# Optimization experiments

Measured on AMD Instinct MI355X. Metric: run time of the kernel, lower is better.

The kernel has to match this reference:

```python
import jax, jax.numpy as jnp
import numpy as np


def grid_sample_bilinear(img, grid):
    """Replicates torch F.grid_sample(mode='bilinear', padding_mode='zeros',
    align_corners=False). img: [B,C,Hin,Win]; grid: [B,Ho,Wo,2] in [-1,1]
    with grid[...,0]=x (width), grid[...,1]=y (height). Returns [B,C,Ho,Wo]."""
    B, C, Hin, Win = img.shape
    x = (grid[..., 0] + 1.0) * (Win * 0.5) - 0.5  # unnormalized pixel coords
    y = (grid[..., 1] + 1.0) * (Hin * 0.5) - 0.5
    x0 = jnp.floor(x)
    y0 = jnp.floor(y)
    wx1 = x - x0
    wy1 = y - y0

    def tap(xi, yi, w):
        valid = ((xi >= 0) & (xi < Win) & (yi >= 0) & (yi < Hin)).astype(img.dtype)
        xc = jnp.clip(xi, 0, Win - 1).astype(jnp.int32)
        yc = jnp.clip(yi, 0, Hin - 1).astype(jnp.int32)
        def gather_one(im, yb, xb, wb):
            return im[:, yb, xb] * wb[None]  # [C,Ho,Wo]
        return jax.vmap(gather_one)(img, yc, xc, valid * w)

    return (tap(x0, y0, (1.0 - wx1) * (1.0 - wy1))
            + tap(x0 + 1.0, y0, wx1 * (1.0 - wy1))
            + tap(x0, y0 + 1.0, (1.0 - wx1) * wy1)
            + tap(x0 + 1.0, y0 + 1.0, wx1 * wy1))


def setup_inputs() -> dict:
    key = jax.random.key(0)
    k_uv, k1, k2, k3, k4 = jax.random.split(key, 5)
    W, H = 2048, 2048
    B, Ho, Wo = 8, 1024, 1024
    return {
        "uv": jax.random.uniform(k_uv, (B, Ho, Wo, 2), dtype=jnp.float32),
        "layer1": jax.random.normal(k1, (1, 1, W, H), dtype=jnp.float32),
        "layer2": jax.random.normal(k2, (1, 1, W // 2, H // 2), dtype=jnp.float32),
        "layer3": jax.random.normal(k3, (1, 1, W // 4, H // 4), dtype=jnp.float32),
        "layer4": jax.random.normal(k4, (1, 1, W // 8, H // 8), dtype=jnp.float32),
    }


def reference(uv, layer1, layer2, layer3, layer4):
    B = uv.shape[0]
    grid = uv * 2.0 - 1.0
    y = None
    for layer in (layer1, layer2, layer3, layer4):
        img = jnp.broadcast_to(layer, (B,) + layer.shape[1:])  # repeat(B,1,1,1)
        s = grid_sample_bilinear(img, grid)
        y = s if y is None else y + s
    return y  # [B,1,Ho,Wo]
```

## Files before the change

### kernel.cpp

```cpp
#include <hip/hip_runtime.h>
#include <hip/hip_fp16.h>


typedef unsigned int u32x2 __attribute__((ext_vector_type(2)));
typedef unsigned int u32x4 __attribute__((ext_vector_type(4)));
typedef float f32x4 __attribute__((ext_vector_type(4)));

#define K 1024
#define CHUNK 4096
#define HB 4096
#define SEG (CHUNK * 256)
#define NXCD 8

__device__ __forceinline__ int binof(float u, float v) {
    int bx = min(max((int)(u * 32.0f), 0), 31);
    int by = min(max((int)(v * 32.0f), 0), 31);
    return by * 32 + bx;
}

__global__ __launch_bounds__(256) void repack_hist_kernel(
    const float* __restrict__ l1, const float* __restrict__ l2,
    const float* __restrict__ l3, const float* __restrict__ l4,
    __half2* __restrict__ r1, __half2* __restrict__ r2,
    __half2* __restrict__ r3, __half2* __restrict__ r4,
    const float2* __restrict__ uv, unsigned* __restrict__ hist, int n) {
    const int n1 = 2048 * 2048, n2 = 1024 * 1024, n3 = 512 * 512, n4 = 256 * 256;
    int i = blockIdx.x * 256 + threadIdx.x;
    {
        const float* __restrict__ src = nullptr;
        __half2* __restrict__ dst = nullptr;
        int S = 0, logS = 0, j = 0;
        if (i < n1) {
            src = l1; dst = r1; S = 2048; logS = 11; j = i;
        } else if (i < n1 + n2) {
            src = l2; dst = r2; S = 1024; logS = 10; j = i - n1;
        } else if (i < n1 + n2 + n3) {
            src = l3; dst = r3; S = 512; logS = 9; j = i - (n1 + n2);
        } else if (i < n1 + n2 + n3 + n4) {
            src = l4; dst = r4; S = 256; logS = 8; j = i - (n1 + n2 + n3);
        }
        if (src) {
            int y = j >> logS;
            float a = src[j];
            float b = src[(y < S - 1) ? (j + S) : j];
            dst[j] = __halves2half2(__float2half(a), __float2half(b));
        }
    }
    if (hist == nullptr) return;
    int base = blockIdx.x * HB;
    if (base >= n) return;
    __shared__ unsigned cnt[K];
    for (int b = threadIdx.x; b < K; b += 256) cnt[b] = 0u;
    __syncthreads();
    int m = min(HB, n - base);
    const f32x4* uv4 = (const f32x4*)(uv + base);
    int npair = m >> 1;
    for (int k2 = threadIdx.x; k2 < npair; k2 += 256) {
        f32x4 q = __builtin_nontemporal_load(&uv4[k2]);
        atomicAdd(&cnt[binof(q.x, q.y)], 1u);
        atomicAdd(&cnt[binof(q.z, q.w)], 1u);
    }
    if ((m & 1) && threadIdx.x == 0) {
        float2 q = uv[base + m - 1];
        atomicAdd(&cnt[binof(q.x, q.y)], 1u);
    }
    __syncthreads();
    int seg = base / SEG;
    unsigned* gh = hist + (size_t)seg * K;
    for (int b = threadIdx.x; b < K; b += 256) {
        unsigned v = cnt[b];
        if (v) atomicAdd(&gh[b], v);
    }
}

__global__ __launch_bounds__(256) void partition_kernel(
    const float2* __restrict__ uv, const unsigned* __restrict__ hist,
    unsigned* __restrict__ cursor, float2* __restrict__ uv_s,
    unsigned* __restrict__ invp, unsigned* __restrict__ idxp, int n,
    int pinned) {
    __shared__ float2 suv[CHUNK];
    __shared__ unsigned short slid[CHUNK];
    __shared__ unsigned cnt[K];
    __shared__ unsigned lbase[K];
    __shared__ unsigned goff[K];
    __shared__ unsigned part[256];
    int t = threadIdx.x;
    int blk = blockIdx.x;
    int c = pinned ? ((blk % NXCD) * (SEG / CHUNK) + blk / NXCD) : blk;
    int cb = c * CHUNK;
    if (cb >= n) return;
    int cnum = min(CHUNK, n - cb);
    int seg = cb / SEG;
    unsigned segstart = (unsigned)((size_t)seg * SEG);

    {
        const f32x4* uv4 = (const f32x4*)(uv + cb);
        int npair = cnum >> 1;
        for (int k2 = t; k2 < npair; k2 += 256) {
            f32x4 q = uv4[k2];
            suv[k2 * 2] = make_float2(q.x, q.y);
            suv[k2 * 2 + 1] = make_float2(q.z, q.w);
        }
        if ((cnum & 1) && t == 0) suv[cnum - 1] = uv[cb + cnum - 1];
    }
    for (int b = t; b < K; b += 256) cnt[b] = 0u;
    __syncthreads();
    for (int k = t; k < cnum; k += 256)
        atomicAdd(&cnt[binof(suv[k].x, suv[k].y)], 1u);
    __syncthreads();
    {
        unsigned v0 = cnt[t * 4], v1 = cnt[t * 4 + 1], v2 = cnt[t * 4 + 2],
                 v3 = cnt[t * 4 + 3];
        unsigned s1 = v0, s2 = v0 + v1, s3 = v0 + v1 + v2;
        part[t] = s3 + v3;
        __syncthreads();
        for (int off = 1; off < 256; off <<= 1) {
            unsigned x = (t >= off) ? part[t - off] : 0u;
            __syncthreads();
            part[t] += x;
            __syncthreads();
        }
        unsigned tb = (t > 0) ? part[t - 1] : 0u;
        lbase[t * 4] = tb;
        lbase[t * 4 + 1] = tb + s1;
        lbase[t * 4 + 2] = tb + s2;
        lbase[t * 4 + 3] = tb + s3;
    }
    __syncthreads();
    {
        const unsigned* h = hist + (size_t)seg * K;
        unsigned v0 = h[t * 4], v1 = h[t * 4 + 1], v2 = h[t * 4 + 2],
                 v3 = h[t * 4 + 3];
        unsigned s1 = v0, s2 = v0 + v1, s3 = v0 + v1 + v2;
        part[t] = s3 + v3;
        __syncthreads();
        for (int off = 1; off < 256; off <<= 1) {
            unsigned x = (t >= off) ? part[t - off] : 0u;
            __syncthreads();
            part[t] += x;
            __syncthreads();
        }
        unsigned tb = (t > 0) ? part[t - 1] : 0u;
        unsigned sbv[4] = {tb, tb + s1, tb + s2, tb + s3};
        for (int j = 0; j < 4; ++j) {
            int b = t * 4 + j;
            unsigned cc = cnt[b];
            unsigned r = cc ? atomicAdd(&cursor[(size_t)seg * K + b], cc) : 0u;
            goff[b] = segstart + sbv[j] + r;
        }
    }
    __syncthreads();
    for (int b = t; b < K; b += 256) cnt[b] = 0u;
    __syncthreads();
    for (int k = t; k < cnum; k += 256) {
        int b = binof(suv[k].x, suv[k].y);
        unsigned r = atomicAdd(&cnt[b], 1u);
        slid[lbase[b] + r] = (unsigned short)k;
        if (invp) invp[cb + k] = goff[b] + r;
    }
    __syncthreads();
    for (int s = t; s < cnum; s += 256) {
        int lid = slid[s];
        float2 q = suv[lid];
        int b = binof(q.x, q.y);
        unsigned pos = goff[b] + ((unsigned)s - lbase[b]);
        uv_s[pos] = q;
        if (idxp) idxp[pos] = (unsigned)(cb + lid);
    }
}

__device__ __forceinline__ float sample_level(const __half2* __restrict__ R,
                                              const int S, const float gx,
                                              const float gy) {
    const float halfS = 0.5f * (float)S;
    float x = (gx + 1.0f) * halfS - 0.5f;
    float y = (gy + 1.0f) * halfS - 0.5f;
    float xf = floorf(x), yf = floorf(y);
    float wx = x - xf, wy = y - yf;
    int x0 = (int)xf, y0 = (int)yf;

    int yc = min(max(y0, 0), S - 1);
    float wa = (y0 >= 0) ? (1.0f - wy) : wy;
    if (y0 < -1 || y0 >= S) wa = 0.0f;
    float wb = (y0 >= 0 && y0 < S - 1) ? wy : 0.0f;

    int xb = min(max(x0, 0), S - 2);
    bool xin = (x0 >= 0) && (x0 <= S - 2);
    float wxa = xin ? (1.0f - wx) : ((x0 == -1) ? wx : 0.0f);
    float wxb = xin ? wx : ((x0 == S - 1) ? (1.0f - wx) : 0.0f);

    uint2 q;
    __builtin_memcpy(&q, (const char*)(R + (size_t)yc * (size_t)S + xb), 8);
    __half2 ca = *(const __half2*)&q.x;
    __half2 cb = *(const __half2*)&q.y;
    float2 fa = __half22float2(ca);
    float2 fb = __half22float2(cb);
    float cola = fmaf(wa, fa.x, wb * fa.y);
    float colb = fmaf(wa, fb.x, wb * fb.y);
    return fmaf(wxa, cola, wxb * colb);
}

__device__ __forceinline__ float sample_point(const __half2* __restrict__ r1,
                                              const __half2* __restrict__ r2,
                                              const __half2* __restrict__ r3,
                                              const __half2* __restrict__ r4,
                                              float ux, float uy) {
    float gx = ux * 2.0f - 1.0f;
    float gy = uy * 2.0f - 1.0f;
    float acc = sample_level(r1, 2048, gx, gy);
    acc += sample_level(r2, 1024, gx, gy);
    acc += sample_level(r3, 512, gx, gy);
    acc += sample_level(r4, 256, gx, gy);
    return acc;
}

__global__ __launch_bounds__(256) void lappyr_sample4(
    const float2* __restrict__ uv_s, const __half2* __restrict__ r1,
    const __half2* __restrict__ r2, const __half2* __restrict__ r3,
    const __half2* __restrict__ r4, float* __restrict__ val_s, int n,
    int pinned) {
    int blk = blockIdx.x;
    int sb = pinned ? ((blk % NXCD) * (SEG / 1024) + blk / NXCD) : blk;
    int base = sb * 1024 + threadIdx.x * 4;
    if (base + 3 < n) {
        const f32x4* u4 = (const f32x4*)(uv_s + base);
        f32x4 a = __builtin_nontemporal_load(u4);
        f32x4 b = __builtin_nontemporal_load(u4 + 1);
        f32x4 res;
        res.x = sample_point(r1, r2, r3, r4, a.x, a.y);
        res.y = sample_point(r1, r2, r3, r4, a.z, a.w);
        res.z = sample_point(r1, r2, r3, r4, b.x, b.y);
        res.w = sample_point(r1, r2, r3, r4, b.z, b.w);
        *(f32x4*)(val_s + base) = res;
    } else {
        for (int j = 0; j < 4; ++j) {
            int p = base + j;
            if (p < n) {
                float2 q = uv_s[p];
                val_s[p] = sample_point(r1, r2, r3, r4, q.x, q.y);
            }
        }
    }
}

__global__ __launch_bounds__(256) void lappyr_unsort4(
    const unsigned* __restrict__ inv, const float* __restrict__ val_s,
    float* __restrict__ out, int n, int pinned) {
    int blk = blockIdx.x;
    int sb = pinned ? ((blk % NXCD) * (SEG / 1024) + blk / NXCD) : blk;
    int base = sb * 1024 + threadIdx.x * 4;
    if (base + 3 < n) {
        u32x4 iv = __builtin_nontemporal_load((const u32x4*)(inv + base));
        f32x4 res;
        res.x = val_s[iv.x];
        res.y = val_s[iv.y];
        res.z = val_s[iv.z];
        res.w = val_s[iv.w];
        __builtin_nontemporal_store(res, (f32x4*)(out + base));
    } else {
        for (int j = 0; j < 4; ++j) {
            int p = base + j;
            if (p < n) out[p] = val_s[inv[p]];
        }
    }
}

__global__ __launch_bounds__(256) void lappyr_sample_sorted(
    const float2* __restrict__ uv_s, const unsigned* __restrict__ idx_s,
    const __half2* __restrict__ r1, const __half2* __restrict__ r2,
    const __half2* __restrict__ r3, const __half2* __restrict__ r4,
    float* __restrict__ out, int n, int pinned) {
    int blk = blockIdx.x;
    int sb = pinned ? ((blk % NXCD) * (SEG / 512) + blk / NXCD) : blk;
    int i = sb * 256 + threadIdx.x;
    int p0 = i * 2;
    if (p0 >= n) return;
    if (p0 + 1 < n) {
        f32x4 q = __builtin_nontemporal_load((const f32x4*)uv_s + i);
        u32x2 id = __builtin_nontemporal_load((const u32x2*)idx_s + i);
        float a0 = sample_point(r1, r2, r3, r4, q.x, q.y);
        float a1 = sample_point(r1, r2, r3, r4, q.z, q.w);
        out[id.x] = a0;
        out[id.y] = a1;
    } else {
        float2 q = uv_s[p0];
        out[idx_s[p0]] = sample_point(r1, r2, r3, r4, q.x, q.y);
    }
}

__global__ __launch_bounds__(256) void lappyr_sample_kernel(
    const float2* __restrict__ uv, const __half2* __restrict__ r1,
    const __half2* __restrict__ r2, const __half2* __restrict__ r3,
    const __half2* __restrict__ r4, float* __restrict__ out, int n) {
    int i = blockIdx.x * blockDim.x + threadIdx.x;
    if (i >= n) return;
    float2 p = uv[i];
    out[i] = sample_point(r1, r2, r3, r4, p.x, p.y);
}

__device__ __forceinline__ float bilin_f32(const float* __restrict__ img,
                                           const int S, const float gx,
                                           const float gy) {
    const float halfS = 0.5f * (float)S;
    float x = (gx + 1.0f) * halfS - 0.5f;
    float y = (gy + 1.0f) * halfS - 0.5f;
    float xf = floorf(x), yf = floorf(y);
    float wx = x - xf, wy = y - yf;
    int x0 = (int)xf, y0 = (int)yf, x1 = x0 + 1, y1 = y0 + 1;
    float ex0 = (x0 >= 0 && x0 < S) ? (1.0f - wx) : 0.0f;
    float ex1 = (x1 >= 0 && x1 < S) ? wx : 0.0f;
    float ey0 = (y0 >= 0 && y0 < S) ? (1.0f - wy) : 0.0f;
    float ey1 = (y1 >= 0 && y1 < S) ? wy : 0.0f;
    int xc0 = min(max(x0, 0), S - 1), xc1 = min(max(x1, 0), S - 1);
    int yc0 = min(max(y0, 0), S - 1), yc1 = min(max(y1, 0), S - 1);
    const float* r0 = img + (size_t)yc0 * S;
    const float* r1 = img + (size_t)yc1 * S;
    return ey0 * fmaf(ex0, r0[xc0], ex1 * r0[xc1]) +
           ey1 * fmaf(ex0, r1[xc0], ex1 * r1[xc1]);
}

__global__ __launch_bounds__(256) void lappyr_f32_kernel(
    const float2* __restrict__ uv, const float* __restrict__ l1,
    const float* __restrict__ l2, const float* __restrict__ l3,
    const float* __restrict__ l4, float* __restrict__ out, int n) {
    int i = blockIdx.x * blockDim.x + threadIdx.x;
    if (i >= n) return;
    float2 p = uv[i];
    float gx = p.x * 2.0f - 1.0f;
    float gy = p.y * 2.0f - 1.0f;
    float acc = bilin_f32(l1, 2048, gx, gy);
    acc += bilin_f32(l2, 1024, gx, gy);
    acc += bilin_f32(l3, 512, gx, gy);
    acc += bilin_f32(l4, 256, gx, gy);
    out[i] = acc;
}

extern "C" void kernel_launch(void* const* d_in, const int* in_sizes, int n_in,
                              void* d_out, int out_size, void* d_ws, size_t ws_size,
                              hipStream_t stream) {
    const float2* uv = (const float2*)d_in[0];
    const float* l1 = (const float*)d_in[1];
    const float* l2 = (const float*)d_in[2];
    const float* l3 = (const float*)d_in[3];
    const float* l4 = (const float*)d_in[4];
    float* out = (float*)d_out;
    int n = out_size;

    const size_t n1 = 2048u * 2048u, n2 = 1024u * 1024u, n3 = 512u * 512u,
                 n4 = 256u * 256u;
    const size_t ntot = n1 + n2 + n3 + n4;
    const size_t rep_bytes = ntot * sizeof(__half2);

    int nseg = (n + SEG - 1) / SEG;
    size_t tbl_bytes = (size_t)nseg * K * 4 * 2;

    size_t off_uvs = (rep_bytes + 255) & ~(size_t)255;
    size_t off_inv = off_uvs + (size_t)n * 8;
    size_t off_val = off_inv + (size_t)n * 4;
    size_t off_hist2 = (off_val + (size_t)n * 4 + 255) & ~(size_t)255;
    size_t need2 = off_hist2 + tbl_bytes;
    size_t off_idx = off_uvs + (size_t)n * 8;
    size_t off_hist1 = (off_idx + (size_t)n * 4 + 255) & ~(size_t)255;
    size_t need1 = off_hist1 + tbl_bytes;

    int repack_blocks = (int)((ntot + 255) / 256);

    if (ws_size >= rep_bytes) {
        char* ws = (char*)d_ws;
        __half2* r1 = (__half2*)ws;
        __half2* r2 = r1 + n1;
        __half2* r3 = r2 + n2;
        __half2* r4 = r3 + n3;
        int pinned = (n == NXCD * SEG) ? 1 : 0;
        int hist_blocks = (n + HB - 1) / HB;
        int ga = max(repack_blocks, hist_blocks);
        int nchunks = (n + CHUNK - 1) / CHUNK;
        if (ws_size >= need2 && n > 0) {
            float2* uv_s = (float2*)(ws + off_uvs);
            unsigned* inv = (unsigned*)(ws + off_inv);
            float* val_s = (float*)(ws + off_val);
            unsigned* hist = (unsigned*)(ws + off_hist2);
            unsigned* cursor = hist + (size_t)nseg * K;
            hipMemsetAsync(ws + off_hist2, 0, tbl_bytes, stream);
            repack_hist_kernel<<<ga, 256, 0, stream>>>(l1, l2, l3, l4, r1, r2, r3,
                                                       r4, uv, hist, n);
            partition_kernel<<<nchunks, 256, 0, stream>>>(
                uv, hist, cursor, uv_s, inv, nullptr, n, pinned);
            int nb4 = (n + 1023) / 1024;
            lappyr_sample4<<<nb4, 256, 0, stream>>>(uv_s, r1, r2, r3, r4, val_s,
                                                    n, pinned);
            lappyr_unsort4<<<nb4, 256, 0, stream>>>(inv, val_s, out, n, pinned);
        } else if (ws_size >= need1 && n > 0) {
            float2* uv_s = (float2*)(ws + off_uvs);
            unsigned* idx_s = (unsigned*)(ws + off_idx);
            unsigned* hist = (unsigned*)(ws + off_hist1);
            unsigned* cursor = hist + (size_t)nseg * K;
            hipMemsetAsync(ws + off_hist1, 0, tbl_bytes, stream);
            repack_hist_kernel<<<ga, 256, 0, stream>>>(l1, l2, l3, l4, r1, r2, r3,
                                                       r4, uv, hist, n);
            partition_kernel<<<nchunks, 256, 0, stream>>>(
                uv, hist, cursor, uv_s, nullptr, idx_s, n, pinned);
            int nh = (n + 1) / 2;
            lappyr_sample_sorted<<<(nh + 255) / 256, 256, 0, stream>>>(
                uv_s, idx_s, r1, r2, r3, r4, out, n, pinned);
        } else {
            repack_hist_kernel<<<repack_blocks, 256, 0, stream>>>(
                l1, l2, l3, l4, r1, r2, r3, r4, uv, nullptr, n);
            lappyr_sample_kernel<<<(n + 255) / 256, 256, 0, stream>>>(
                uv, r1, r2, r3, r4, out, n);
        }
    } else {
        lappyr_f32_kernel<<<(n + 255) / 256, 256, 0, stream>>>(uv, l1, l2, l3, l4,
                                                               out, n);
    }
}
```

Before: 312.5 us.

## Precompute segment bin offsets with a scan kernel and streamline partition

Adds a per-segment scan kernel that turns the global histogram into starting cursors, so the partition kernel no longer rescans the histogram itself. The partition kernel now counts straight from global uv, scatters full uv pairs into a shared sorted buffer and writes the inverse permutation as vector stores. This removes the extra shared-memory uv copy and the local-id indirection. It costs one extra kernel launch and a second global read of uv per chunk.

```diff
diff --git a/kernel.cpp b/kernel.cpp
--- a/kernel.cpp
+++ b/kernel.cpp
@@ -73,11 +73,121 @@
     }
 }
 
+__global__ __launch_bounds__(256) void scan_kernel(
+    const unsigned* __restrict__ hist, unsigned* __restrict__ cursor) {
+    int seg = blockIdx.x;
+    const unsigned* h = hist + (size_t)seg * K;
+    unsigned* c = cursor + (size_t)seg * K;
+    __shared__ unsigned part[256];
+    int t = threadIdx.x;
+    unsigned v0 = h[t * 4], v1 = h[t * 4 + 1], v2 = h[t * 4 + 2], v3 = h[t * 4 + 3];
+    unsigned s1 = v0, s2 = v0 + v1, s3 = v0 + v1 + v2;
+    part[t] = s3 + v3;
+    __syncthreads();
+    for (int off = 1; off < 256; off <<= 1) {
+        unsigned x = (t >= off) ? part[t - off] : 0u;
+        __syncthreads();
+        part[t] += x;
+        __syncthreads();
+    }
+    unsigned tb = (t > 0) ? part[t - 1] : 0u;
+    unsigned segstart = (unsigned)((size_t)seg * SEG);
+    c[t * 4] = segstart + tb;
+    c[t * 4 + 1] = segstart + tb + s1;
+    c[t * 4 + 2] = segstart + tb + s2;
+    c[t * 4 + 3] = segstart + tb + s3;
+}
+
 __global__ __launch_bounds__(256) void partition_kernel(
+    const float2* __restrict__ uv, unsigned* __restrict__ cursor,
+    float2* __restrict__ uv_s, unsigned* __restrict__ invp, int n, int pinned) {
+    __shared__ float2 ssort[CHUNK];
+    __shared__ unsigned cnt[K];
+    __shared__ unsigned lbase[K];
+    __shared__ unsigned gdiff[K];
+    __shared__ unsigned part[256];
+    int t = threadIdx.x;
+    int blk = blockIdx.x;
+    int c = pinned ? ((blk % NXCD) * (SEG / CHUNK) + blk / NXCD) : blk;
+    int cb = c * CHUNK;
+    if (cb >= n) return;
+    int cnum = min(CHUNK, n - cb);
+    int seg = cb / SEG;
+
+    for (int b = t; b < K; b += 256) cnt[b] = 0u;
+    __syncthreads();
+    const f32x4* uv4 = (const f32x4*)(uv + cb);
+    int npair = cnum >> 1;
+    for (int k2 = t; k2 < npair; k2 += 256) {
+        f32x4 q = uv4[k2];
+        atomicAdd(&cnt[binof(q.x, q.y)], 1u);
+        atomicAdd(&cnt[binof(q.z, q.w)], 1u);
+    }
+    if ((cnum & 1) && t == 0) {
+        float2 q = uv[cb + cnum - 1];
+        atomicAdd(&cnt[binof(q.x, q.y)], 1u);
+    }
+    __syncthreads();
+    {
+        unsigned v0 = cnt[t * 4], v1 = cnt[t * 4 + 1], v2 = cnt[t * 4 + 2],
+                 v3 = cnt[t * 4 + 3];
+        unsigned s1 = v0, s2 = v0 + v1, s3 = v0 + v1 + v2;
+        part[t] = s3 + v3;
+        __syncthreads();
+        for (int off = 1; off < 256; off <<= 1) {
+            unsigned x = (t >= off) ? part[t - off] : 0u;
+            __syncthreads();
+            part[t] += x;
+            __syncthreads();
+        }
+        unsigned tb = (t > 0) ? part[t - 1] : 0u;
+        unsigned lb[4] = {tb, tb + s1, tb + s2, tb + s3};
+        unsigned cv[4] = {v0, v1, v2, v3};
+        for (int j = 0; j < 4; ++j) {
+            int b = t * 4 + j;
+            lbase[b] = lb[j];
+            unsigned goff =
+                cv[j] ? atomicAdd(&cursor[(size_t)seg * K + b], cv[j]) : 0u;
+            gdiff[b] = goff - lb[j];
+        }
+    }
+    __syncthreads();
+    for (int b = t; b < K; b += 256) cnt[b] = 0u;
+    __syncthreads();
+    for (int k2 = t; k2 < npair; k2 += 256) {
+        f32x4 q = uv4[k2];
+        int ba = binof(q.x, q.y);
+        unsigned sa = lbase[ba] + atomicAdd(&cnt[ba], 1u);
+        ssort[sa] = make_float2(q.x, q.y);
+        int bb = binof(q.z, q.w);
+        unsigned sb = lbase[bb] + atomicAdd(&cnt[bb], 1u);
+        ssort[sb] = make_float2(q.z, q.w);
+        if (invp) {
+            u32x2 iv;
+            iv.x = gdiff[ba] + sa;
+            iv.y = gdiff[bb] + sb;
+            *(u32x2*)(invp + cb + k2 * 2) = iv;
+        }
+    }
+    if ((cnum & 1) && t == 0) {
+        float2 q = uv[cb + cnum - 1];
+        int b = binof(q.x, q.y);
+        unsigned s = lbase[b] + atomicAdd(&cnt[b], 1u);
+        ssort[s] = q;
+        if (invp) invp[cb + cnum - 1] = gdiff[b] + s;
+    }
+    __syncthreads();
+    for (int s = t; s < cnum; s += 256) {
+        float2 q = ssort[s];
+        int b = binof(q.x, q.y);
+        uv_s[gdiff[b] + (unsigned)s] = q;
+    }
+}
+
+__global__ __launch_bounds__(256) void partition_idx_kernel(
     const float2* __restrict__ uv, const unsigned* __restrict__ hist,
     unsigned* __restrict__ cursor, float2* __restrict__ uv_s,
-    unsigned* __restrict__ invp, unsigned* __restrict__ idxp, int n,
-    int pinned) {
+    unsigned* __restrict__ idxp, int n, int pinned) {
     __shared__ float2 suv[CHUNK];
     __shared__ unsigned short slid[CHUNK];
     __shared__ unsigned cnt[K];
@@ -92,7 +202,6 @@
     int cnum = min(CHUNK, n - cb);
     int seg = cb / SEG;
     unsigned segstart = (unsigned)((size_t)seg * SEG);
-
     {
         const f32x4* uv4 = (const f32x4*)(uv + cb);
         int npair = cnum >> 1;
@@ -156,7 +265,6 @@
         int b = binof(suv[k].x, suv[k].y);
         unsigned r = atomicAdd(&cnt[b], 1u);
         slid[lbase[b] + r] = (unsigned short)k;
-        if (invp) invp[cb + k] = goff[b] + r;
     }
     __syncthreads();
     for (int s = t; s < cnum; s += 256) {
@@ -165,7 +273,7 @@
         int b = binof(q.x, q.y);
         unsigned pos = goff[b] + ((unsigned)s - lbase[b]);
         uv_s[pos] = q;
-        if (idxp) idxp[pos] = (unsigned)(cb + lid);
+        idxp[pos] = (unsigned)(cb + lid);
     }
 }
 
@@ -381,11 +489,12 @@
             float* val_s = (float*)(ws + off_val);
             unsigned* hist = (unsigned*)(ws + off_hist2);
             unsigned* cursor = hist + (size_t)nseg * K;
-            hipMemsetAsync(ws + off_hist2, 0, tbl_bytes, stream);
+            hipMemsetAsync(hist, 0, (size_t)nseg * K * 4, stream);
             repack_hist_kernel<<<ga, 256, 0, stream>>>(l1, l2, l3, l4, r1, r2, r3,
                                                        r4, uv, hist, n);
-            partition_kernel<<<nchunks, 256, 0, stream>>>(
-                uv, hist, cursor, uv_s, inv, nullptr, n, pinned);
+            scan_kernel<<<nseg, 256, 0, stream>>>(hist, cursor);
+            partition_kernel<<<nchunks, 256, 0, stream>>>(uv, cursor, uv_s, inv,
+                                                          n, pinned);
             int nb4 = (n + 1023) / 1024;
             lappyr_sample4<<<nb4, 256, 0, stream>>>(uv_s, r1, r2, r3, r4, val_s,
                                                     n, pinned);
@@ -395,11 +504,11 @@
             unsigned* idx_s = (unsigned*)(ws + off_idx);
             unsigned* hist = (unsigned*)(ws + off_hist1);
             unsigned* cursor = hist + (size_t)nseg * K;
-            hipMemsetAsync(ws + off_hist1, 0, tbl_bytes, stream);
+            hipMemsetAsync(hist, 0, tbl_bytes, stream);
             repack_hist_kernel<<<ga, 256, 0, stream>>>(l1, l2, l3, l4, r1, r2, r3,
                                                        r4, uv, hist, n);
-            partition_kernel<<<nchunks, 256, 0, stream>>>(
-                uv, hist, cursor, uv_s, nullptr, idx_s, n, pinned);
+            partition_idx_kernel<<<nchunks, 256, 0, stream>>>(
+                uv, hist, cursor, uv_s, idx_s, n, pinned);
             int nh = (n + 1) / 2;
             lappyr_sample_sorted<<<(nh + 255) / 256, 256, 0, stream>>>(
                 uv_s, idx_s, r1, r2, r3, r4, out, n, pinned);
```

New measurement: 312.3 us. About the same (-0.0%).

## Replace atomic segment histogram with per-chunk histograms and precomputed cursor scan

Applied to the files above, without the earlier changes.

Each partition chunk now gets its own histogram written by the repack kernel. A new cursor kernel prefix-scans these histograms per segment, so every chunk gets a deterministic global offset and the global atomics and the memset are no longer needed. The partition kernel skips recounting the bins, does a single scatter into shared memory using wave-shuffle scans, and writes the inverse indices in vectorized form. The repack also processes four elements per thread with vector loads. In exchange there is an extra serial-ish cursor launch with large per-chunk tables, chunk size drops to 2048, and the fallback sorted-sample path is removed.

```diff
diff --git a/kernel.cpp b/kernel.cpp
--- a/kernel.cpp
+++ b/kernel.cpp
@@ -7,15 +7,50 @@
 typedef float f32x4 __attribute__((ext_vector_type(4)));
 
 #define K 1024
-#define CHUNK 4096
-#define HB 4096
-#define SEG (CHUNK * 256)
+#define CHUNK 2048
+#define CPS 512
+#define SEG (CHUNK * CPS)
 #define NXCD 8
 
 __device__ __forceinline__ int binof(float u, float v) {
     int bx = min(max((int)(u * 32.0f), 0), 31);
     int by = min(max((int)(v * 32.0f), 0), 31);
     return by * 32 + bx;
+}
+
+__device__ __forceinline__ unsigned pack2(float lo, float hi) {
+    __half2 h = __halves2half2(__float2half(lo), __float2half(hi));
+    unsigned w;
+    __builtin_memcpy(&w, &h, 4);
+    return w;
+}
+
+__device__ __forceinline__ void repack_item(
+    const float* __restrict__ l1, const float* __restrict__ l2,
+    const float* __restrict__ l3, const float* __restrict__ l4,
+    __half2* __restrict__ r1, __half2* __restrict__ r2,
+    __half2* __restrict__ r3, __half2* __restrict__ r4, int e) {
+    const int n1 = 2048 * 2048, n2 = 1024 * 1024, n3 = 512 * 512, n4 = 256 * 256;
+    const float* __restrict__ src = nullptr;
+    __half2* __restrict__ dst = nullptr;
+    int S = 0, logS = 0, j = 0;
+    if (e < n1) {
+        src = l1; dst = r1; S = 2048; logS = 11; j = e;
+    } else if (e < n1 + n2) {
+        src = l2; dst = r2; S = 1024; logS = 10; j = e - n1;
+    } else if (e < n1 + n2 + n3) {
+        src = l3; dst = r3; S = 512; logS = 9; j = e - (n1 + n2);
+    } else if (e < n1 + n2 + n3 + n4) {
+        src = l4; dst = r4; S = 256; logS = 8; j = e - (n1 + n2 + n3);
+    }
+    if (src) {
+        int y = j >> logS;
+        f32x4 a = *(const f32x4*)(src + j);
+        f32x4 b = *(const f32x4*)(src + ((y < S - 1) ? (j + S) : j));
+        u32x4 o = {pack2(a.x, b.x), pack2(a.y, b.y), pack2(a.z, b.z),
+                   pack2(a.w, b.w)};
+        *(u32x4*)(dst + j) = o;
+    }
 }
 
 __global__ __launch_bounds__(256) void repack_hist_kernel(
@@ -23,149 +58,144 @@
     const float* __restrict__ l3, const float* __restrict__ l4,
     __half2* __restrict__ r1, __half2* __restrict__ r2,
     __half2* __restrict__ r3, __half2* __restrict__ r4,
-    const float2* __restrict__ uv, unsigned* __restrict__ hist, int n) {
-    const int n1 = 2048 * 2048, n2 = 1024 * 1024, n3 = 512 * 512, n4 = 256 * 256;
-    int i = blockIdx.x * 256 + threadIdx.x;
-    {
-        const float* __restrict__ src = nullptr;
-        __half2* __restrict__ dst = nullptr;
-        int S = 0, logS = 0, j = 0;
-        if (i < n1) {
-            src = l1; dst = r1; S = 2048; logS = 11; j = i;
-        } else if (i < n1 + n2) {
-            src = l2; dst = r2; S = 1024; logS = 10; j = i - n1;
-        } else if (i < n1 + n2 + n3) {
-            src = l3; dst = r3; S = 512; logS = 9; j = i - (n1 + n2);
-        } else if (i < n1 + n2 + n3 + n4) {
-            src = l4; dst = r4; S = 256; logS = 8; j = i - (n1 + n2 + n3);
-        }
-        if (src) {
-            int y = j >> logS;
-            float a = src[j];
-            float b = src[(y < S - 1) ? (j + S) : j];
-            dst[j] = __halves2half2(__float2half(a), __float2half(b));
-        }
-    }
-    if (hist == nullptr) return;
-    int base = blockIdx.x * HB;
+    const float2* __restrict__ uv, unsigned* __restrict__ chist, int n) {
+    repack_item(l1, l2, l3, l4, r1, r2, r3, r4,
+                (blockIdx.x * 256 + threadIdx.x) * 4);
+    if (chist == nullptr) return;
+    int c = blockIdx.x;
+    int base = c * CHUNK;
     if (base >= n) return;
     __shared__ unsigned cnt[K];
-    for (int b = threadIdx.x; b < K; b += 256) cnt[b] = 0u;
+    int t = threadIdx.x;
+    for (int b = t; b < K; b += 256) cnt[b] = 0u;
     __syncthreads();
-    int m = min(HB, n - base);
+    int m = min(CHUNK, n - base);
     const f32x4* uv4 = (const f32x4*)(uv + base);
     int npair = m >> 1;
-    for (int k2 = threadIdx.x; k2 < npair; k2 += 256) {
+    for (int k2 = t; k2 < npair; k2 += 256) {
         f32x4 q = __builtin_nontemporal_load(&uv4[k2]);
         atomicAdd(&cnt[binof(q.x, q.y)], 1u);
         atomicAdd(&cnt[binof(q.z, q.w)], 1u);
     }
-    if ((m & 1) && threadIdx.x == 0) {
+    if ((m & 1) && t == 0) {
         float2 q = uv[base + m - 1];
         atomicAdd(&cnt[binof(q.x, q.y)], 1u);
     }
     __syncthreads();
-    int seg = base / SEG;
-    unsigned* gh = hist + (size_t)seg * K;
-    for (int b = threadIdx.x; b < K; b += 256) {
-        unsigned v = cnt[b];
-        if (v) atomicAdd(&gh[b], v);
+    for (int b = t; b < K; b += 256) chist[(size_t)c * K + b] = cnt[b];
+}
+
+__global__ __launch_bounds__(1024) void cursor2_kernel(
+    const unsigned* __restrict__ chist, unsigned* __restrict__ cursor,
+    int nchunks) {
+    int seg = blockIdx.x;
+    int b = threadIdx.x;
+    int c0 = seg * CPS;
+    unsigned tot = 0;
+    for (int c = 0; c < CPS; ++c) {
+        int cc = c0 + c;
+        if (cc < nchunks) tot += chist[(size_t)cc * K + b];
+    }
+    unsigned incl = tot;
+    int lane = b & 63, wave = b >> 6;
+    for (int d = 1; d < 64; d <<= 1) {
+        unsigned y = __shfl_up(incl, d);
+        if (lane >= d) incl += y;
+    }
+    __shared__ unsigned wtot[16];
+    if (lane == 63) wtot[wave] = incl;
+    __syncthreads();
+    unsigned wpre = 0;
+    for (int w = 0; w < 16; ++w)
+        if (w < wave) wpre += wtot[w];
+    unsigned run = (unsigned)seg * (unsigned)SEG + wpre + (incl - tot);
+    for (int c = 0; c < CPS; ++c) {
+        cursor[((size_t)seg * CPS + c) * K + b] = run;
+        int cc = c0 + c;
+        if (cc < nchunks) run += chist[(size_t)cc * K + b];
     }
 }
 
 __global__ __launch_bounds__(256) void partition_kernel(
-    const float2* __restrict__ uv, const unsigned* __restrict__ hist,
-    unsigned* __restrict__ cursor, float2* __restrict__ uv_s,
-    unsigned* __restrict__ invp, unsigned* __restrict__ idxp, int n,
-    int pinned) {
-    __shared__ float2 suv[CHUNK];
-    __shared__ unsigned short slid[CHUNK];
+    const float2* __restrict__ uv, const unsigned* __restrict__ chist,
+    const unsigned* __restrict__ cursor, float2* __restrict__ uv_s,
+    unsigned* __restrict__ invp, int n, int pinned) {
+    __shared__ float2 ssort[CHUNK];
     __shared__ unsigned cnt[K];
     __shared__ unsigned lbase[K];
-    __shared__ unsigned goff[K];
-    __shared__ unsigned part[256];
+    __shared__ unsigned gdiff[K];
+    __shared__ unsigned wsum[4];
     int t = threadIdx.x;
     int blk = blockIdx.x;
-    int c = pinned ? ((blk % NXCD) * (SEG / CHUNK) + blk / NXCD) : blk;
+    int c = pinned ? ((blk % NXCD) * CPS + blk / NXCD) : blk;
     int cb = c * CHUNK;
     if (cb >= n) return;
     int cnum = min(CHUNK, n - cb);
-    int seg = cb / SEG;
-    unsigned segstart = (unsigned)((size_t)seg * SEG);
-
+    int seg = c / CPS;
+    int cidx = c % CPS;
+
+    u32x4 hv = *(const u32x4*)(chist + (size_t)c * K + t * 4);
     {
-        const f32x4* uv4 = (const f32x4*)(uv + cb);
-        int npair = cnum >> 1;
-        for (int k2 = t; k2 < npair; k2 += 256) {
-            f32x4 q = uv4[k2];
-            suv[k2 * 2] = make_float2(q.x, q.y);
-            suv[k2 * 2 + 1] = make_float2(q.z, q.w);
+        unsigned s1 = hv.x, s2 = hv.x + hv.y, s3 = hv.x + hv.y + hv.z;
+        unsigned tot = s3 + hv.w;
+        unsigned incl = tot;
+        int lane = t & 63, wave = t >> 6;
+        for (int d = 1; d < 64; d <<= 1) {
+            unsigned y = __shfl_up(incl, d);
+            if (lane >= d) incl += y;
         }
-        if ((cnum & 1) && t == 0) suv[cnum - 1] = uv[cb + cnum - 1];
-    }
-    for (int b = t; b < K; b += 256) cnt[b] = 0u;
+        if (lane == 63) wsum[wave] = incl;
+        __syncthreads();
+        unsigned wpre = 0;
+        for (int w = 0; w < 4; ++w)
+            if (w < wave) wpre += wsum[w];
+        unsigned tb = wpre + (incl - tot);
+        const unsigned* crow = cursor + ((size_t)seg * CPS + cidx) * K;
+        u32x4 cv = *(const u32x4*)(crow + t * 4);
+        unsigned lb0 = tb, lb1 = tb + s1, lb2 = tb + s2, lb3 = tb + s3;
+        lbase[t * 4] = lb0;
+        lbase[t * 4 + 1] = lb1;
+        lbase[t * 4 + 2] = lb2;
+        lbase[t * 4 + 3] = lb3;
+        gdiff[t * 4] = cv.x - lb0;
+        gdiff[t * 4 + 1] = cv.y - lb1;
+        gdiff[t * 4 + 2] = cv.z - lb2;
+        gdiff[t * 4 + 3] = cv.w - lb3;
+        cnt[t * 4] = 0u;
+        cnt[t * 4 + 1] = 0u;
+        cnt[t * 4 + 2] = 0u;
+        cnt[t * 4 + 3] = 0u;
+    }
     __syncthreads();
-    for (int k = t; k < cnum; k += 256)
-        atomicAdd(&cnt[binof(suv[k].x, suv[k].y)], 1u);
-    __syncthreads();
-    {
-        unsigned v0 = cnt[t * 4], v1 = cnt[t * 4 + 1], v2 = cnt[t * 4 + 2],
-                 v3 = cnt[t * 4 + 3];
-        unsigned s1 = v0, s2 = v0 + v1, s3 = v0 + v1 + v2;
-        part[t] = s3 + v3;
-        __syncthreads();
-        for (int off = 1; off < 256; off <<= 1) {
-            unsigned x = (t >= off) ? part[t - off] : 0u;
-            __syncthreads();
-            part[t] += x;
-            __syncthreads();
+    const f32x4* uv4 = (const f32x4*)(uv + cb);
+    int npair = cnum >> 1;
+    for (int k2 = t; k2 < npair; k2 += 256) {
+        f32x4 q = uv4[k2];
+        int ba = binof(q.x, q.y);
+        unsigned sa = lbase[ba] + atomicAdd(&cnt[ba], 1u);
+        ssort[sa] = make_float2(q.x, q.y);
+        int bb = binof(q.z, q.w);
+        unsigned sb = lbase[bb] + atomicAdd(&cnt[bb], 1u);
+        ssort[sb] = make_float2(q.z, q.w);
+        if (invp) {
+            u32x2 iv;
+            iv.x = gdiff[ba] + sa;
+            iv.y = gdiff[bb] + sb;
+            __builtin_nontemporal_store(iv, (u32x2*)(invp + cb + k2 * 2));
         }
-        unsigned tb = (t > 0) ? part[t - 1] : 0u;
-        lbase[t * 4] = tb;
-        lbase[t * 4 + 1] = tb + s1;
-        lbase[t * 4 + 2] = tb + s2;
-        lbase[t * 4 + 3] = tb + s3;
-    }
-    __syncthreads();
-    {
-        const unsigned* h = hist + (size_t)seg * K;
-        unsigned v0 = h[t * 4], v1 = h[t * 4 + 1], v2 = h[t * 4 + 2],
-                 v3 = h[t * 4 + 3];
-        unsigned s1 = v0, s2 = v0 + v1, s3 = v0 + v1 + v2;
-        part[t] = s3 + v3;
-        __syncthreads();
-        for (int off = 1; off < 256; off <<= 1) {
-            unsigned x = (t >= off) ? part[t - off] : 0u;
-            __syncthreads();
-            part[t] += x;
-            __syncthreads();
-        }
-        unsigned tb = (t > 0) ? part[t - 1] : 0u;
-        unsigned sbv[4] = {tb, tb + s1, tb + s2, tb + s3};
-        for (int j = 0; j < 4; ++j) {
-            int b = t * 4 + j;
-            unsigned cc = cnt[b];
-            unsigned r = cc ? atomicAdd(&cursor[(size_t)seg * K + b], cc) : 0u;
-            goff[b] = segstart + sbv[j] + r;
-        }
-    }
-    __syncthreads();
-    for (int b = t; b < K; b += 256) cnt[b] = 0u;
-    __syncthreads();
-    for (int k = t; k < cnum; k += 256) {
-        int b = binof(suv[k].x, suv[k].y);
-        unsigned r = atomicAdd(&cnt[b], 1u);
-        slid[lbase[b] + r] = (unsigned short)k;
-        if (invp) invp[cb + k] = goff[b] + r;
+    }
+    if ((cnum & 1) && t == 0) {
+        float2 q = uv[cb + cnum - 1];
+        int b = binof(q.x, q.y);
+        unsigned s = lbase[b] + atomicAdd(&cnt[b], 1u);
+        ssort[s] = q;
+        if (invp) invp[cb + cnum - 1] = gdiff[b] + s;
     }
     __syncthreads();
     for (int s = t; s < cnum; s += 256) {
-        int lid = slid[s];
-        float2 q = suv[lid];
+        float2 q = ssort[s];
         int b = binof(q.x, q.y);
-        unsigned pos = goff[b] + ((unsigned)s - lbase[b]);
-        uv_s[pos] = q;
-        if (idxp) idxp[pos] = (unsigned)(cb + lid);
+        uv_s[gdiff[b] + (unsigned)s] = q;
     }
 }
 
@@ -265,29 +295,6 @@
     }
 }
 
-__global__ __launch_bounds__(256) void lappyr_sample_sorted(
-    const float2* __restrict__ uv_s, const unsigned* __restrict__ idx_s,
-    const __half2* __restrict__ r1, const __half2* __restrict__ r2,
-    const __half2* __restrict__ r3, const __half2* __restrict__ r4,
-    float* __restrict__ out, int n, int pinned) {
-    int blk = blockIdx.x;
-    int sb = pinned ? ((blk % NXCD) * (SEG / 512) + blk / NXCD) : blk;
-    int i = sb * 256 + threadIdx.x;
-    int p0 = i * 2;
-    if (p0 >= n) return;
-    if (p0 + 1 < n) {
-        f32x4 q = __builtin_nontemporal_load((const f32x4*)uv_s + i);
-        u32x2 id = __builtin_nontemporal_load((const u32x2*)idx_s + i);
-        float a0 = sample_point(r1, r2, r3, r4, q.x, q.y);
-        float a1 = sample_point(r1, r2, r3, r4, q.z, q.w);
-        out[id.x] = a0;
-        out[id.y] = a1;
-    } else {
-        float2 q = uv_s[p0];
-        out[idx_s[p0]] = sample_point(r1, r2, r3, r4, q.x, q.y);
-    }
-}
-
 __global__ __launch_bounds__(256) void lappyr_sample_kernel(
     const float2* __restrict__ uv, const __half2* __restrict__ r1,
     const __half2* __restrict__ r2, const __half2* __restrict__ r3,
@@ -352,18 +359,18 @@
     const size_t rep_bytes = ntot * sizeof(__half2);
 
     int nseg = (n + SEG - 1) / SEG;
-    size_t tbl_bytes = (size_t)nseg * K * 4 * 2;
+    int nchunks = (n + CHUNK - 1) / CHUNK;
+
+    size_t chist_b = (size_t)nseg * CPS * K * 4;
+    size_t tbl = chist_b * 2;
+    size_t val_region = ((size_t)n * 4 > tbl) ? (size_t)n * 4 : tbl;
 
     size_t off_uvs = (rep_bytes + 255) & ~(size_t)255;
     size_t off_inv = off_uvs + (size_t)n * 8;
-    size_t off_val = off_inv + (size_t)n * 4;
-    size_t off_hist2 = (off_val + (size_t)n * 4 + 255) & ~(size_t)255;
-    size_t need2 = off_hist2 + tbl_bytes;
-    size_t off_idx = off_uvs + (size_t)n * 8;
-    size_t off_hist1 = (off_idx + (size_t)n * 4 + 255) & ~(size_t)255;
-    size_t need1 = off_hist1 + tbl_bytes;
-
-    int repack_blocks = (int)((ntot + 255) / 256);
+    size_t off_val = (off_inv + (size_t)n * 4 + 255) & ~(size_t)255;
+    size_t need2 = off_val + val_region;
+
+    int repack_blocks = (int)((ntot / 4 + 255) / 256);
 
     if (ws_size >= rep_bytes) {
         char* ws = (char*)d_ws;
@@ -372,37 +379,22 @@
         __half2* r3 = r2 + n2;
         __half2* r4 = r3 + n3;
         int pinned = (n == NXCD * SEG) ? 1 : 0;
-        int hist_blocks = (n + HB - 1) / HB;
-        int ga = max(repack_blocks, hist_blocks);
-        int nchunks = (n + CHUNK - 1) / CHUNK;
         if (ws_size >= need2 && n > 0) {
             float2* uv_s = (float2*)(ws + off_uvs);
             unsigned* inv = (unsigned*)(ws + off_inv);
             float* val_s = (float*)(ws + off_val);
-            unsigned* hist = (unsigned*)(ws + off_hist2);
-            unsigned* cursor = hist + (size_t)nseg * K;
-            hipMemsetAsync(ws + off_hist2, 0, tbl_bytes, stream);
-            repack_hist_kernel<<<ga, 256, 0, stream>>>(l1, l2, l3, l4, r1, r2, r3,
-                                                       r4, uv, hist, n);
-            partition_kernel<<<nchunks, 256, 0, stream>>>(
-                uv, hist, cursor, uv_s, inv, nullptr, n, pinned);
+            unsigned* chist = (unsigned*)(ws + off_val);
+            unsigned* cursor = (unsigned*)(ws + off_val + chist_b);
+            int ga = max(repack_blocks, nchunks);
+            repack_hist_kernel<<<ga, 256, 0, stream>>>(l1, l2, l3, l4, r1, r2,
+                                                       r3, r4, uv, chist, n);
+            cursor2_kernel<<<nseg, 1024, 0, stream>>>(chist, cursor, nchunks);
+            partition_kernel<<<nchunks, 256, 0, stream>>>(uv, chist, cursor,
+                                                          uv_s, inv, n, pinned);
             int nb4 = (n + 1023) / 1024;
             lappyr_sample4<<<nb4, 256, 0, stream>>>(uv_s, r1, r2, r3, r4, val_s,
                                                     n, pinned);
             lappyr_unsort4<<<nb4, 256, 0, stream>>>(inv, val_s, out, n, pinned);
-        } else if (ws_size >= need1 && n > 0) {
-            float2* uv_s = (float2*)(ws + off_uvs);
-            unsigned* idx_s = (unsigned*)(ws + off_idx);
-            unsigned* hist = (unsigned*)(ws + off_hist1);
-            unsigned* cursor = hist + (size_t)nseg * K;
-            hipMemsetAsync(ws + off_hist1, 0, tbl_bytes, stream);
-            repack_hist_kernel<<<ga, 256, 0, stream>>>(l1, l2, l3, l4, r1, r2, r3,
-                                                       r4, uv, hist, n);
-            partition_kernel<<<nchunks, 256, 0, stream>>>(
-                uv, hist, cursor, uv_s, nullptr, idx_s, n, pinned);
-            int nh = (n + 1) / 2;
-            lappyr_sample_sorted<<<(nh + 255) / 256, 256, 0, stream>>>(
-                uv_s, idx_s, r1, r2, r3, r4, out, n, pinned);
         } else {
             repack_hist_kernel<<<repack_blocks, 256, 0, stream>>>(
                 l1, l2, l3, l4, r1, r2, r3, r4, uv, nullptr, n);
```

Result: slower. 512.4 us (+64.0%).
